# Kernel tuning notes

Hardware: AMD Instinct MI355X
Metric: run time of the kernel (lower is better)

Reference implementation:

```python
import jax, jax.numpy as jnp
import numpy as np

VOCAB = 100000
N_NODES = 200000
D = 128


def setup_inputs() -> dict:
    key = jax.random.key(0)
    k1, k2, k3, k4, k5, k6 = jax.random.split(key, 6)
    nodes = jax.random.randint(k1, (N_NODES,), 0, VOCAB, dtype=jnp.int64 if jax.config.jax_enable_x64 else jnp.int32).astype(jnp.int32)
    c2e_weight = jax.random.normal(k2, (VOCAB, D), dtype=jnp.float32)
    w1 = jax.random.normal(k3, (D, D), dtype=jnp.float32) * (1.0 / np.sqrt(D))
    b1 = jax.random.normal(k4, (D,), dtype=jnp.float32) * 0.01
    w2 = jax.random.normal(k5, (D, D), dtype=jnp.float32) * (1.0 / np.sqrt(D))
    b2 = jax.random.normal(k6, (D,), dtype=jnp.float32) * 0.01
    return {"nodes": nodes, "c2e_weight": c2e_weight, "w1": w1, "b1": b1, "w2": w2, "b2": b2}


def reference(nodes, c2e_weight, w1, b1, w2, b2):
    # Vectorized version of the per-node Python loop:
    #   ce = c2e.weight[node]; x = relu(w_r1(ce)); out = relu(w_r2(x))
    ce = c2e_weight[nodes]                         # [N, D] gather
    h = jax.nn.relu(ce @ w1.T + b1)                # [N, D]
    out = jax.nn.relu(h @ w2.T + b2)               # [N, D]
    return out
```

## Files before the change

kernel.cpp:

```cpp
#include <hip/hip_runtime.h>
#include <hip/hip_bf16.h>

#define D_DIM   128
#define MT      64
#define NBLOCKS 512

typedef __attribute__((ext_vector_type(8))) short bf16x8;
typedef __attribute__((ext_vector_type(4))) float f32x4;

__device__ __forceinline__ unsigned short f2bf(float f) {
    return __builtin_bit_cast(unsigned short, __float2bfloat16(f));
}

__device__ __forceinline__ int sw_off(int row, int col) {
    return row * 128 + ((((col >> 3) ^ (row & 15)) << 3) | (col & 7));
}

__device__ __forceinline__ void stage_w(const float* __restrict__ w,
                                        unsigned short* __restrict__ sW, int t) {
    #pragma unroll
    for (int i = 0; i < 8; ++i) {
        const int idx4 = i * 512 + t;
        const float4 v = ((const float4*)w)[idx4];
        const int row = idx4 >> 5;
        const int c4  = (idx4 & 31) * 4;
        ushort4 b;
        b.x = f2bf(v.x); b.y = f2bf(v.y); b.z = f2bf(v.z); b.w = f2bf(v.w);
        *(ushort4*)&sW[sw_off(row, c4)] = b;
    }
}

__global__ __launch_bounds__(512, 4)
void ctx_encoder(const int* __restrict__ nodes,
                 const float* __restrict__ c2e,
                 const float* __restrict__ w1,
                 const float* __restrict__ b1,
                 const float* __restrict__ w2,
                 const float* __restrict__ b2,
                 float* __restrict__ out,
                 int N) {
    __shared__ unsigned short sW1[D_DIM * 128];
    __shared__ unsigned short sW2[D_DIM * 128];
    __shared__ unsigned short sH [MT   * 128];

    const int t    = threadIdx.x;
    const int lane = t & 63;
    const int wave = t >> 6;
    const int pair = wave >> 1;
    const int half = wave & 1;
    const int cl   = lane & 15;
    const int quad = lane >> 4;

    stage_w(w1, sW1, t);
    stage_w(w2, sW2, t);

    float bias1[4], bias2[4];
    #pragma unroll
    for (int c = 0; c < 4; ++c) {
        const int j = (half * 4 + c) * 16 + cl;
        bias1[c] = b1[j];
        bias2[c] = b2[j];
    }

    const int nTiles = (N + MT - 1) / MT;
    const int myrow  = pair * 16 + cl;
    int tl = blockIdx.x;

    int r0 = tl * MT + myrow;            r0 = r0 < N ? r0 : N - 1;
    int idx_cur = nodes[r0];
    int idx_nxt = 0;
    if (tl + NBLOCKS < nTiles) {
        int r1 = (tl + NBLOCKS) * MT + myrow;  r1 = r1 < N ? r1 : N - 1;
        idx_nxt = nodes[r1];
    }

    float4 g[8];
    {
        const float* rowp = c2e + (size_t)idx_cur * D_DIM + quad * 8;
        #pragma unroll
        for (int ks = 0; ks < 4; ++ks) {
            g[2 * ks]     = *(const float4*)(rowp + ks * 32);
            g[2 * ks + 1] = *(const float4*)(rowp + ks * 32 + 4);
        }
    }
    __syncthreads();

    while (tl < nTiles) {
        bf16x8 aF[4];
        #pragma unroll
        for (int ks = 0; ks < 4; ++ks) {
            bf16x8 a;
            a[0] = (short)f2bf(g[2 * ks].x);     a[1] = (short)f2bf(g[2 * ks].y);
            a[2] = (short)f2bf(g[2 * ks].z);     a[3] = (short)f2bf(g[2 * ks].w);
            a[4] = (short)f2bf(g[2 * ks + 1].x); a[5] = (short)f2bf(g[2 * ks + 1].y);
            a[6] = (short)f2bf(g[2 * ks + 1].z); a[7] = (short)f2bf(g[2 * ks + 1].w);
            aF[ks] = a;
        }

        const int tn = tl + NBLOCKS;
        if (tn < nTiles) {
            const float* rowp = c2e + (size_t)idx_nxt * D_DIM + quad * 8;
            #pragma unroll
            for (int ks = 0; ks < 4; ++ks) {
                g[2 * ks]     = *(const float4*)(rowp + ks * 32);
                g[2 * ks + 1] = *(const float4*)(rowp + ks * 32 + 4);
            }
            if (tn + NBLOCKS < nTiles) {
                int rn = (tn + NBLOCKS) * MT + myrow;  rn = rn < N ? rn : N - 1;
                idx_nxt = nodes[rn];
            }
        }

        #pragma unroll
        for (int c = 0; c < 4; ++c) {
            const int ct = half * 4 + c;
            bf16x8 bF[4];
            #pragma unroll
            for (int ks = 0; ks < 4; ++ks)
                bF[ks] = *(const bf16x8*)&sW1[sw_off(ct * 16 + cl, ks * 32 + quad * 8)];
            f32x4 acc = {0.f, 0.f, 0.f, 0.f};
            #pragma unroll
            for (int ks = 0; ks < 4; ++ks)
                acc = __builtin_amdgcn_mfma_f32_16x16x32_bf16(aF[ks], bF[ks], acc, 0, 0, 0);
            const int j = ct * 16 + cl;
            #pragma unroll
            for (int r = 0; r < 4; ++r) {
                float h = acc[r] + bias1[c];
                h = h > 0.f ? h : 0.f;
                sH[sw_off(pair * 16 + quad * 4 + r, j)] = f2bf(h);
            }
        }
        __syncthreads();

        bf16x8 hF[4];
        #pragma unroll
        for (int ks = 0; ks < 4; ++ks)
            hF[ks] = *(const bf16x8*)&sH[sw_off(pair * 16 + cl, ks * 32 + quad * 8)];

        const size_t obase = (size_t)tl * MT;
        #pragma unroll
        for (int c = 0; c < 4; ++c) {
            const int ct = half * 4 + c;
            bf16x8 bF[4];
            #pragma unroll
            for (int ks = 0; ks < 4; ++ks)
                bF[ks] = *(const bf16x8*)&sW2[sw_off(ct * 16 + cl, ks * 32 + quad * 8)];
            f32x4 acc = {0.f, 0.f, 0.f, 0.f};
            #pragma unroll
            for (int ks = 0; ks < 4; ++ks)
                acc = __builtin_amdgcn_mfma_f32_16x16x32_bf16(hF[ks], bF[ks], acc, 0, 0, 0);
            const int j = ct * 16 + cl;
            #pragma unroll
            for (int r = 0; r < 4; ++r) {
                float o = acc[r] + bias2[c];
                o = o > 0.f ? o : 0.f;
                const long grow = (long)(obase + pair * 16 + quad * 4 + r);
                if (grow < N)
                    out[(size_t)grow * D_DIM + j] = o;
            }
        }
        __syncthreads();

        tl += NBLOCKS;
    }
}

extern "C" void kernel_launch(void* const* d_in, const int* in_sizes, int n_in,
                              void* d_out, int out_size, void* d_ws, size_t ws_size,
                              hipStream_t stream) {
    const int*   nodes = (const int*)d_in[0];
    const float* c2e   = (const float*)d_in[1];
    const float* w1    = (const float*)d_in[2];
    const float* b1    = (const float*)d_in[3];
    const float* w2    = (const float*)d_in[4];
    const float* b2    = (const float*)d_in[5];
    float* out = (float*)d_out;
    const int N = in_sizes[0];

    ctx_encoder<<<dim3(NBLOCKS), dim3(512), 0, stream>>>(nodes, c2e, w1, b1, w2, b2, out, N);
}
```

Before: 185.3 us.

## Gather embedding rows coalesced via LDS staging and reuse one shared buffer

Each group of 8 threads now loads one full embedding row with contiguous float4 reads, converts it to bf16 and writes it into a swizzled shared tile. The MFMA A fragments are then read from that tile instead of each lane fetching strided pieces of a row. The same shared buffer also holds the hidden activations, and the barriers are moved to fit this reuse. This aims at better-coalesced gather traffic, at the cost of extra LDS writes, an additional barrier per tile, and launch bounds relaxed from 4 to 2 waves per SIMD, which frees registers but may lower occupancy.

Result: faster. 164.9 us (-11.0%).

```diff
diff --git a/kernel.cpp b/kernel.cpp
--- a/kernel.cpp
+++ b/kernel.cpp
@@ -4,6 +4,7 @@
 #define D_DIM   128
 #define MT      64
 #define NBLOCKS 512
+#define NTHR    512
 
 typedef __attribute__((ext_vector_type(8))) short bf16x8;
 typedef __attribute__((ext_vector_type(4))) float f32x4;
@@ -20,7 +21,7 @@
                                         unsigned short* __restrict__ sW, int t) {
     #pragma unroll
     for (int i = 0; i < 8; ++i) {
-        const int idx4 = i * 512 + t;
+        const int idx4 = i * NTHR + t;
         const float4 v = ((const float4*)w)[idx4];
         const int row = idx4 >> 5;
         const int c4  = (idx4 & 31) * 4;
@@ -30,7 +31,7 @@
     }
 }
 
-__global__ __launch_bounds__(512, 4)
+__global__ __launch_bounds__(NTHR, 2)
 void ctx_encoder(const int* __restrict__ nodes,
                  const float* __restrict__ c2e,
                  const float* __restrict__ w1,
@@ -41,7 +42,7 @@
                  int N) {
     __shared__ unsigned short sW1[D_DIM * 128];
     __shared__ unsigned short sW2[D_DIM * 128];
-    __shared__ unsigned short sH [MT   * 128];
+    __shared__ unsigned short sX [MT    * 128];
 
     const int t    = threadIdx.x;
     const int lane = t & 63;
@@ -50,6 +51,9 @@
     const int half = wave & 1;
     const int cl   = lane & 15;
     const int quad = lane >> 4;
+
+    const int grow0 = t >> 3;
+    const int gc    = t & 7;
 
     stage_w(w1, sW1, t);
     stage_w(w2, sW2, t);
@@ -63,53 +67,51 @@
     }
 
     const int nTiles = (N + MT - 1) / MT;
-    const int myrow  = pair * 16 + cl;
     int tl = blockIdx.x;
 
-    int r0 = tl * MT + myrow;            r0 = r0 < N ? r0 : N - 1;
+    int r0 = tl * MT + grow0;  r0 = r0 < N ? r0 : N - 1;
     int idx_cur = nodes[r0];
+    float4 g[4];
+    {
+        const float* rp = c2e + (size_t)idx_cur * D_DIM + gc * 4;
+        #pragma unroll
+        for (int i = 0; i < 4; ++i)
+            g[i] = *(const float4*)(rp + i * 32);
+    }
     int idx_nxt = 0;
     if (tl + NBLOCKS < nTiles) {
-        int r1 = (tl + NBLOCKS) * MT + myrow;  r1 = r1 < N ? r1 : N - 1;
+        int r1 = (tl + NBLOCKS) * MT + grow0;  r1 = r1 < N ? r1 : N - 1;
         idx_nxt = nodes[r1];
-    }
-
-    float4 g[8];
-    {
-        const float* rowp = c2e + (size_t)idx_cur * D_DIM + quad * 8;
-        #pragma unroll
-        for (int ks = 0; ks < 4; ++ks) {
-            g[2 * ks]     = *(const float4*)(rowp + ks * 32);
-            g[2 * ks + 1] = *(const float4*)(rowp + ks * 32 + 4);
-        }
     }
     __syncthreads();
 
     while (tl < nTiles) {
+        #pragma unroll
+        for (int i = 0; i < 4; ++i) {
+            ushort4 b;
+            b.x = f2bf(g[i].x); b.y = f2bf(g[i].y);
+            b.z = f2bf(g[i].z); b.w = f2bf(g[i].w);
+            *(ushort4*)&sX[sw_off(grow0, gc * 4 + i * 32)] = b;
+        }
+        __syncthreads();
+
         bf16x8 aF[4];
         #pragma unroll
-        for (int ks = 0; ks < 4; ++ks) {
-            bf16x8 a;
-            a[0] = (short)f2bf(g[2 * ks].x);     a[1] = (short)f2bf(g[2 * ks].y);
-            a[2] = (short)f2bf(g[2 * ks].z);     a[3] = (short)f2bf(g[2 * ks].w);
-            a[4] = (short)f2bf(g[2 * ks + 1].x); a[5] = (short)f2bf(g[2 * ks + 1].y);
-            a[6] = (short)f2bf(g[2 * ks + 1].z); a[7] = (short)f2bf(g[2 * ks + 1].w);
-            aF[ks] = a;
-        }
+        for (int ks = 0; ks < 4; ++ks)
+            aF[ks] = *(const bf16x8*)&sX[sw_off(pair * 16 + cl, ks * 32 + quad * 8)];
 
         const int tn = tl + NBLOCKS;
         if (tn < nTiles) {
-            const float* rowp = c2e + (size_t)idx_nxt * D_DIM + quad * 8;
+            const float* rp = c2e + (size_t)idx_nxt * D_DIM + gc * 4;
             #pragma unroll
-            for (int ks = 0; ks < 4; ++ks) {
-                g[2 * ks]     = *(const float4*)(rowp + ks * 32);
-                g[2 * ks + 1] = *(const float4*)(rowp + ks * 32 + 4);
-            }
+            for (int i = 0; i < 4; ++i)
+                g[i] = *(const float4*)(rp + i * 32);
             if (tn + NBLOCKS < nTiles) {
-                int rn = (tn + NBLOCKS) * MT + myrow;  rn = rn < N ? rn : N - 1;
+                int rn = (tn + NBLOCKS) * MT + grow0;  rn = rn < N ? rn : N - 1;
                 idx_nxt = nodes[rn];
             }
         }
+        __syncthreads();
 
         #pragma unroll
         for (int c = 0; c < 4; ++c) {
@@ -127,7 +129,7 @@
             for (int r = 0; r < 4; ++r) {
                 float h = acc[r] + bias1[c];
                 h = h > 0.f ? h : 0.f;
-                sH[sw_off(pair * 16 + quad * 4 + r, j)] = f2bf(h);
+                sX[sw_off(pair * 16 + quad * 4 + r, j)] = f2bf(h);
             }
         }
         __syncthreads();
@@ -135,7 +137,8 @@
         bf16x8 hF[4];
         #pragma unroll
         for (int ks = 0; ks < 4; ++ks)
-            hF[ks] = *(const bf16x8*)&sH[sw_off(pair * 16 + cl, ks * 32 + quad * 8)];
+            hF[ks] = *(const bf16x8*)&sX[sw_off(pair * 16 + cl, ks * 32 + quad * 8)];
+        __syncthreads();
 
         const size_t obase = (size_t)tl * MT;
         #pragma unroll
@@ -159,7 +162,6 @@
                     out[(size_t)grow * D_DIM + j] = o;
             }
         }
-        __syncthreads();
 
         tl += NBLOCKS;
     }
@@ -177,5 +179,5 @@
     float* out = (float*)d_out;
     const int N = in_sizes[0];
 
-    ctx_encoder<<<dim3(NBLOCKS), dim3(512), 0, stream>>>(nodes, c2e, w1, b1, w2, b2, out, N);
+    ctx_encoder<<<dim3(NBLOCKS), dim3(NTHR), 0, stream>>>(nodes, c2e, w1, b1, w2, b2, out, N);
 }
```
